# Performance work log

Measured on AMD Instinct MI355X. Metric: run time of the kernel, lower is better.

## Reference

```python
import jax, jax.numpy as jnp
import numpy as np

H_HEADS = 16
STATE_N = 64

def setup_inputs() -> dict:
    key = jax.random.key(0)
    ks = jax.random.split(key, 9)
    B, T, D = 2, 1024, 1024
    H, ch, N = H_HEADS, D // H_HEADS, STATE_N
    inp = jax.random.normal(ks[0], (B, T, D), dtype=jnp.float32)
    # lin_logA params scaled so exp(cumsum(logA)) stays bounded (decaying state)
    W_logA = jax.random.normal(ks[1], (H, 1, ch), dtype=jnp.float32) * 0.01
    b_logA = jnp.full((H, 1), -0.05, dtype=jnp.float32)
    W_XBC = jax.random.normal(ks[3], (H, ch + 2 * N, ch), dtype=jnp.float32) * (1.0 / np.sqrt(ch))
    b_XBC = jax.random.normal(ks[4], (H, ch + 2 * N), dtype=jnp.float32) * 0.02
    W_gate = jax.random.normal(ks[5], (H, ch, ch), dtype=jnp.float32) * (1.0 / np.sqrt(ch))
    b_gate = jax.random.normal(ks[6], (H, ch), dtype=jnp.float32) * 0.02
    W_out = jax.random.normal(ks[7], (D, D), dtype=jnp.float32) * (1.0 / np.sqrt(D))
    b_out = jax.random.normal(ks[8], (D,), dtype=jnp.float32) * 0.02
    return {"inp": inp, "W_logA": W_logA, "b_logA": b_logA, "W_XBC": W_XBC,
            "b_XBC": b_XBC, "W_gate": W_gate, "b_gate": b_gate,
            "W_out": W_out, "b_out": b_out}

def _mamba2_forward(inp, W_logA, b_logA, W_XBC, b_XBC, W_gate, b_gate, W_out, b_out):
    B, T, D = inp.shape
    H, N = H_HEADS, STATE_N
    ch = D // H
    x = inp.reshape(B, T, H, ch)  # B,T,H,ch
    # MultiheadLinear: matmul((H,out,in), x[...,None]) + bias
    logA = jnp.einsum('hoc,bthc->btho', W_logA, x)[..., 0] + b_logA[:, 0]  # B,T,H
    XBC = jax.nn.silu(jnp.einsum('hoc,bthc->btho', W_XBC, x) + b_XBC)     # B,T,H,ch+2N
    X = XBC[..., :ch]                 # B,T,H,ch
    Bm = XBC[..., ch:ch + N]          # B,T,H,N
    Cm = XBC[..., ch + N:]            # B,T,H,N
    # quadratic SSM: A_ss[b,h,i,j] = exp(cum[i]-cum[j]) for j<=i else 0
    cum = jnp.cumsum(jnp.swapaxes(logA, 1, 2), axis=-1)  # B,H,T
    diff = cum[..., :, None] - cum[..., None, :]          # B,H,T,T
    causal = jnp.tril(jnp.ones((T, T), dtype=bool))
    A_ss = jnp.where(causal, jnp.exp(jnp.where(causal, diff, 0.0)), 0.0)  # B,H,T,T
    G = jnp.einsum('bihn,bjhn->bhij', Cm, Bm)             # B,H,T,T (C_i . B_j)
    Y = jnp.einsum('bhij,bjhc->bihc', A_ss * G, X)        # B,T,H,ch
    gate = jnp.einsum('hoc,bthc->btho', W_gate, x) + b_gate
    Yg = (gate * Y).reshape(B, T, D)
    return Yg @ W_out.T + b_out

def reference(inp, W_logA, b_logA, W_XBC, b_XBC, W_gate, b_gate, W_out, b_out):
    return _mamba2_forward(inp, W_logA, b_logA, W_XBC, b_XBC, W_gate, b_gate, W_out, b_out)
```

## Files before the change

kernel.cpp:

```cpp
#include <hip/hip_runtime.h>

typedef unsigned int   u32;
typedef unsigned short u16;
typedef __attribute__((ext_vector_type(8))) short bf16x8;
typedef __attribute__((ext_vector_type(4))) float f32x4;

__device__ __forceinline__ float bfs(u16 u) {
  union { u32 i; float f; } v; v.i = ((u32)u) << 16; return v.f;
}
__device__ __forceinline__ u16 f2bf(float f) {
  union { float f; u32 i; } v; v.f = f;
  u32 r = v.i + 0x7fffu + ((v.i >> 16) & 1u);
  return (u16)(r >> 16);
}
__device__ __forceinline__ ushort4 f2bf4(float4 v) {
  ushort4 p; p.x = f2bf(v.x); p.y = f2bf(v.y); p.z = f2bf(v.z); p.w = f2bf(v.w);
  return p;
}

__global__ __launch_bounds__(256) void k_proj(
    const float* __restrict__ inp,
    const float* __restrict__ W_XBC,  const float* __restrict__ b_XBC,
    const float* __restrict__ W_gate, const float* __restrict__ b_gate,
    const float* __restrict__ W_logA, const float* __restrict__ b_logA,
    u16* __restrict__ XsT, u16* __restrict__ Bms, u16* __restrict__ Cms,
    u16* __restrict__ gates, float* __restrict__ logAs)
{
  int tt = blockIdx.x, h = blockIdx.y;
  int tid = threadIdx.x;
  int w = tid >> 6, l = tid & 63, q = l >> 4, lr = l & 15;
  int m0 = tt * 64;
  int b = m0 >> 10, tl0 = m0 & 1023;
  int bh = b * 16 + h;

  __shared__ u16 Xt[64][72];
  __shared__ u16 Wt[256][72];
  __shared__ float wl[64];

  if (tid < 64) wl[tid] = W_logA[h * 64 + tid];
#pragma unroll
  for (int i = 0; i < 4; ++i) {
    int f = tid + 256 * i; int r = f >> 4, cq = f & 15;
    float4 xv = *(const float4*)(inp + (size_t)(m0 + r) * 1024 + h * 64 + 4 * cq);
    *(ushort4*)&Xt[r][4 * cq] = f2bf4(xv);
  }
#pragma unroll
  for (int i = 0; i < 16; ++i) {
    int f = tid + 256 * i; int r = f >> 4, cq = f & 15;
    const float* wsrc = (r < 192) ? (W_XBC + ((size_t)h * 192 + r) * 64)
                                  : (W_gate + ((size_t)h * 64 + (r - 192)) * 64);
    *(ushort4*)&Wt[r][4 * cq] = f2bf4(*(const float4*)(wsrc + 4 * cq));
  }
  __syncthreads();

  bf16x8 af[4][2];
#pragma unroll
  for (int rt = 0; rt < 4; ++rt) {
    af[rt][0] = *(const bf16x8*)&Xt[16 * rt + lr][q * 8];
    af[rt][1] = *(const bf16x8*)&Xt[16 * rt + lr][32 + q * 8];
  }

  f32x4 acc[4][4];
#pragma unroll
  for (int rt = 0; rt < 4; ++rt)
#pragma unroll
    for (int ct = 0; ct < 4; ++ct) acc[rt][ct] = (f32x4){0.f, 0.f, 0.f, 0.f};

#pragma unroll
  for (int ct = 0; ct < 4; ++ct) {
    bf16x8 b0 = *(const bf16x8*)&Wt[64 * w + 16 * ct + lr][q * 8];
    bf16x8 b1 = *(const bf16x8*)&Wt[64 * w + 16 * ct + lr][32 + q * 8];
#pragma unroll
    for (int rt = 0; rt < 4; ++rt) {
      acc[rt][ct] = __builtin_amdgcn_mfma_f32_16x16x32_bf16(af[rt][0], b0, acc[rt][ct], 0, 0, 0);
      acc[rt][ct] = __builtin_amdgcn_mfma_f32_16x16x32_bf16(af[rt][1], b1, acc[rt][ct], 0, 0, 0);
    }
  }

  if (tid < 64) {
    float a = b_logA[h];
#pragma unroll 16
    for (int k = 0; k < 64; ++k) a += bfs(Xt[tid][k]) * wl[k];
    logAs[(size_t)bh * 1024 + tl0 + tid] = a;
  }

  if (w == 0) {
#pragma unroll
    for (int ct = 0; ct < 4; ++ct) {
      int n = 16 * ct + lr;
      float bias = b_XBC[h * 192 + n];
#pragma unroll
      for (int rt = 0; rt < 4; ++rt) {
        float4 v;
#pragma unroll
        for (int r = 0; r < 4; ++r) {
          float s = acc[rt][ct][r] + bias;
          (&v.x)[r] = s / (1.f + __expf(-s));
        }
        *(ushort4*)(XsT + ((size_t)bh * 64 + n) * 1024 + tl0 + 16 * rt + q * 4) = f2bf4(v);
      }
    }
  } else if (w < 3) {
    u16* dst = (w == 1) ? Bms : Cms;
    int nbase = h * 192 + 64 * w;
#pragma unroll
    for (int ct = 0; ct < 4; ++ct) {
      int n = 16 * ct + lr;
      float bias = b_XBC[nbase + n];
#pragma unroll
      for (int rt = 0; rt < 4; ++rt)
#pragma unroll
        for (int r = 0; r < 4; ++r) {
          int tloc = tl0 + 16 * rt + q * 4 + r;
          float s = acc[rt][ct][r] + bias;
          s = s / (1.f + __expf(-s));
          dst[((size_t)bh * 1024 + tloc) * 64 + n] = f2bf(s);
        }
    }
  } else {
#pragma unroll
    for (int ct = 0; ct < 4; ++ct) {
      int n = 16 * ct + lr;
      float bias = b_gate[h * 64 + n];
#pragma unroll
      for (int rt = 0; rt < 4; ++rt)
#pragma unroll
        for (int r = 0; r < 4; ++r) {
          int tg = m0 + 16 * rt + q * 4 + r;
          gates[((size_t)tg * 16 + h) * 64 + n] = f2bf(acc[rt][ct][r] + bias);
        }
    }
  }
}

__global__ __launch_bounds__(1024) void k_scan(
    const float* __restrict__ logAs, float* __restrict__ rowexp,
    float* __restrict__ colexp)
{
  int bh = blockIdx.x;
  int t = threadIdx.x;
  int wv = t >> 6, ln = t & 63;
  __shared__ float wsum[16];
  float v = logAs[(size_t)bh * 1024 + t];
#pragma unroll
  for (int off = 1; off < 64; off <<= 1) {
    float n = __shfl_up(v, off, 64);
    if (ln >= off) v += n;
  }
  if (ln == 63) wsum[wv] = v;
  __syncthreads();
  if (wv == 0) {
    float s = (ln < 16) ? wsum[ln] : 0.f;
#pragma unroll
    for (int off = 1; off < 16; off <<= 1) {
      float n = __shfl_up(s, off, 64);
      if (ln >= off) s += n;
    }
    if (ln < 16) wsum[ln] = s;
  }
  __syncthreads();
  if (wv > 0) v += wsum[wv - 1];
  rowexp[(size_t)bh * 1024 + t] = __expf(v);
  colexp[(size_t)bh * 1024 + t] = __expf(-v);
}

__global__ __launch_bounds__(256) void k_wconv(
    const float* __restrict__ Wout, u16* __restrict__ WoutB)
{
  int i = blockIdx.x * 256 + threadIdx.x;
  float4 v = ((const float4*)Wout)[i];
  ((ushort4*)WoutB)[i] = f2bf4(v);
}

__global__ __launch_bounds__(256) void k_ssm(
    const u16* __restrict__ XsT, const u16* __restrict__ Bms, const u16* __restrict__ Cms,
    const float* __restrict__ rowexp, const float* __restrict__ colexp,
    const u16* __restrict__ gates, u16* __restrict__ Yg)
{
  int g = blockIdx.x >> 5;
  int bh = blockIdx.x & 31;
  int it = (g & 1) ? (g >> 1) : (15 - (g >> 1));
  int b = bh >> 4, h = bh & 15;

  const u16* Xb = XsT + (size_t)bh * 64 * 1024;
  const u16* Bb = Bms + (size_t)bh * 1024 * 64;
  const u16* Cb = Cms + (size_t)bh * 1024 * 64;

  int tid = threadIdx.x;
  int w = tid >> 6, l = tid & 63, q = l >> 4, lr = l & 15;

  __shared__ u16 Cts[64][72];
  __shared__ u16 Bts[64][72];
  __shared__ u16 Xts[64][72];
  __shared__ u16 Sts[64][72];
  __shared__ float ref_[64], cef[64];

  int i0 = it * 64;
#pragma unroll
  for (int i = 0; i < 4; ++i) {
    int f = tid + 256 * i; int r = f >> 4, cq = f & 15;
    *(ushort4*)&Cts[r][4 * cq] = *(const ushort4*)(Cb + (size_t)(i0 + r) * 64 + 4 * cq);
  }
  if (tid < 64) ref_[tid] = rowexp[(size_t)bh * 1024 + i0 + tid];
  __syncthreads();

  bf16x8 ca0 = *(const bf16x8*)&Cts[16 * w + lr][q * 8];
  bf16x8 ca1 = *(const bf16x8*)&Cts[16 * w + lr][32 + q * 8];

  f32x4 acc[4];
#pragma unroll
  for (int ct = 0; ct < 4; ++ct) acc[ct] = (f32x4){0.f, 0.f, 0.f, 0.f};

  ushort4 pb[4], px[4]; float pce = 0.f;
#pragma unroll
  for (int i = 0; i < 4; ++i) {
    int f = tid + 256 * i; int r = f >> 4, cq = f & 15;
    pb[i] = *(const ushort4*)(Bb + (size_t)r * 64 + 4 * cq);
    px[i] = *(const ushort4*)(Xb + (size_t)r * 1024 + 4 * cq);
  }
  if (tid < 64) pce = colexp[(size_t)bh * 1024 + tid];

  for (int jt = 0; jt <= it; ++jt) {
    __syncthreads();
#pragma unroll
    for (int i = 0; i < 4; ++i) {
      int f = tid + 256 * i; int r = f >> 4, cq = f & 15;
      *(ushort4*)&Bts[r][4 * cq] = pb[i];
      *(ushort4*)&Xts[r][4 * cq] = px[i];
    }
    if (tid < 64) cef[tid] = pce;
    __syncthreads();

    if (jt < it) {
      int j1 = (jt + 1) * 64;
#pragma unroll
      for (int i = 0; i < 4; ++i) {
        int f = tid + 256 * i; int r = f >> 4, cq = f & 15;
        pb[i] = *(const ushort4*)(Bb + (size_t)(j1 + r) * 64 + 4 * cq);
        px[i] = *(const ushort4*)(Xb + (size_t)r * 1024 + j1 + 4 * cq);
      }
      if (tid < 64) pce = colexp[(size_t)bh * 1024 + j1 + tid];
    }

    bool diag = (jt == it);
#pragma unroll
    for (int ct = 0; ct < 4; ++ct) {
      f32x4 s = (f32x4){0.f, 0.f, 0.f, 0.f};
      bf16x8 b0 = *(const bf16x8*)&Bts[16 * ct + lr][q * 8];
      bf16x8 b1 = *(const bf16x8*)&Bts[16 * ct + lr][32 + q * 8];
      s = __builtin_amdgcn_mfma_f32_16x16x32_bf16(ca0, b0, s, 0, 0, 0);
      s = __builtin_amdgcn_mfma_f32_16x16x32_bf16(ca1, b1, s, 0, 0, 0);
      int jl = 16 * ct + lr;
      float cj = cef[jl];
#pragma unroll
      for (int r = 0; r < 4; ++r) {
        int il = 16 * w + q * 4 + r;
        float v = (diag && jl > il) ? 0.f : s[r] * ref_[il] * cj;
        Sts[il][jl] = f2bf(v);
      }
    }

    bf16x8 sa0 = *(const bf16x8*)&Sts[16 * w + lr][q * 8];
    bf16x8 sa1 = *(const bf16x8*)&Sts[16 * w + lr][32 + q * 8];
#pragma unroll
    for (int ct = 0; ct < 4; ++ct) {
      bf16x8 x0 = *(const bf16x8*)&Xts[16 * ct + lr][q * 8];
      bf16x8 x1 = *(const bf16x8*)&Xts[16 * ct + lr][32 + q * 8];
      acc[ct] = __builtin_amdgcn_mfma_f32_16x16x32_bf16(sa0, x0, acc[ct], 0, 0, 0);
      acc[ct] = __builtin_amdgcn_mfma_f32_16x16x32_bf16(sa1, x1, acc[ct], 0, 0, 0);
    }
  }

#pragma unroll
  for (int ct = 0; ct < 4; ++ct) {
    int c = 16 * ct + lr;
#pragma unroll
    for (int r = 0; r < 4; ++r) {
      int tg = i0 + 16 * w + q * 4 + r;
      size_t row = (size_t)(b * 1024 + tg);
      float gt = bfs(gates[(row * 16 + h) * 64 + c]);
      Yg[row * 1024 + h * 64 + c] = f2bf(acc[ct][r] * gt);
    }
  }
}

__global__ __launch_bounds__(512) void k_out(
    const u16* __restrict__ Yg, const u16* __restrict__ WoutB,
    const float* __restrict__ bout, float* __restrict__ out)
{
  int bm = blockIdx.x, bn = blockIdx.y;
  int tid = threadIdx.x;
  int w = tid >> 6, l = tid & 63, q = l >> 4, lr = l & 15;
  int m0 = bm * 128, d0 = bn * 64;

  __shared__ u16 Yt[128][72];
  __shared__ u16 Wt[64][72];

  f32x4 acc[4];
#pragma unroll
  for (int ct = 0; ct < 4; ++ct) acc[ct] = (f32x4){0.f, 0.f, 0.f, 0.f};

  ushort4 py[4], pw[2];
#pragma unroll
  for (int i = 0; i < 4; ++i) {
    int f = tid + 512 * i; int r = f >> 4, cq = f & 15;
    py[i] = *(const ushort4*)(Yg + (size_t)(m0 + r) * 1024 + 4 * cq);
  }
#pragma unroll
  for (int i = 0; i < 2; ++i) {
    int f = tid + 512 * i; int r = f >> 4, cq = f & 15;
    pw[i] = *(const ushort4*)(WoutB + (size_t)(d0 + r) * 1024 + 4 * cq);
  }

  for (int kt = 0; kt < 16; ++kt) {
    __syncthreads();
#pragma unroll
    for (int i = 0; i < 4; ++i) {
      int f = tid + 512 * i; int r = f >> 4, cq = f & 15;
      *(ushort4*)&Yt[r][4 * cq] = py[i];
    }
#pragma unroll
    for (int i = 0; i < 2; ++i) {
      int f = tid + 512 * i; int r = f >> 4, cq = f & 15;
      *(ushort4*)&Wt[r][4 * cq] = pw[i];
    }
    __syncthreads();

    if (kt < 15) {
      int k1 = (kt + 1) * 64;
#pragma unroll
      for (int i = 0; i < 4; ++i) {
        int f = tid + 512 * i; int r = f >> 4, cq = f & 15;
        py[i] = *(const ushort4*)(Yg + (size_t)(m0 + r) * 1024 + k1 + 4 * cq);
      }
#pragma unroll
      for (int i = 0; i < 2; ++i) {
        int f = tid + 512 * i; int r = f >> 4, cq = f & 15;
        pw[i] = *(const ushort4*)(WoutB + (size_t)(d0 + r) * 1024 + k1 + 4 * cq);
      }
    }

    bf16x8 a0 = *(const bf16x8*)&Yt[16 * w + lr][q * 8];
    bf16x8 a1 = *(const bf16x8*)&Yt[16 * w + lr][32 + q * 8];
#pragma unroll
    for (int ct = 0; ct < 4; ++ct) {
      bf16x8 b0 = *(const bf16x8*)&Wt[16 * ct + lr][q * 8];
      bf16x8 b1 = *(const bf16x8*)&Wt[16 * ct + lr][32 + q * 8];
      acc[ct] = __builtin_amdgcn_mfma_f32_16x16x32_bf16(a0, b0, acc[ct], 0, 0, 0);
      acc[ct] = __builtin_amdgcn_mfma_f32_16x16x32_bf16(a1, b1, acc[ct], 0, 0, 0);
    }
  }

#pragma unroll
  for (int ct = 0; ct < 4; ++ct) {
    int d = d0 + 16 * ct + lr;
    float bo = bout[d];
#pragma unroll
    for (int r = 0; r < 4; ++r) {
      int m = m0 + 16 * w + q * 4 + r;
      out[(size_t)m * 1024 + d] = acc[ct][r] + bo;
    }
  }
}

extern "C" void kernel_launch(void* const* d_in, const int* in_sizes, int n_in,
                              void* d_out, int out_size, void* d_ws, size_t ws_size,
                              hipStream_t stream)
{
  const float* inp   = (const float*)d_in[0];
  const float* WlogA = (const float*)d_in[1];
  const float* blogA = (const float*)d_in[2];
  const float* WXBC  = (const float*)d_in[3];
  const float* bXBC  = (const float*)d_in[4];
  const float* Wgate = (const float*)d_in[5];
  const float* bgate = (const float*)d_in[6];
  const float* Wout  = (const float*)d_in[7];
  const float* bout  = (const float*)d_in[8];
  float* out = (float*)d_out;

  const size_t SZ = (size_t)2 * 16 * 1024 * 64;
  float* logAs  = (float*)d_ws;
  float* rowexp = logAs + 32768;
  float* colexp = rowexp + 32768;
  u16* base16  = (u16*)(colexp + 32768);
  u16* XsT   = base16;
  u16* Bms   = XsT + SZ;
  u16* Cms   = Bms + SZ;
  u16* gates = Cms + SZ;
  u16* Yg    = gates + SZ;
  u16* WoutB = Yg + SZ;

  k_proj<<<dim3(32, 16), 256, 0, stream>>>(inp, WXBC, bXBC, Wgate, bgate,
                                           WlogA, blogA, XsT, Bms, Cms, gates, logAs);
  k_scan<<<32, 1024, 0, stream>>>(logAs, rowexp, colexp);
  k_wconv<<<1024, 256, 0, stream>>>(Wout, WoutB);
  k_ssm<<<dim3(512), 256, 0, stream>>>(XsT, Bms, Cms, rowexp, colexp, gates, Yg);
  k_out<<<dim3(16, 16), 512, 0, stream>>>(Yg, WoutB, bout, out);
}
```

Before: 128.9 us.

## Replace quadratic SSM with chunked state-passing scan (intra-chunk plus inter-chunk states)

Replaces the quadratic causal attention-style SSM loop over all previous chunks with a chunked formulation. Per-chunk states B^T·(colexp·X) are computed, prefix-summed across chunks, and then each chunk combines a diagonal-block term with C·H_prev scaled by rowexp. k_proj also writes a transposed copy of B, and the W_out bf16 conversion is folded into the scan kernel to save a launch. This removes the O(T^2) work and the load imbalance of the triangular loop, at the cost of two extra launches, an fp32 state buffer, a serial 16-step prefix kernel, and bf16 rounding of states that may grow from the unbounded colexp factor.

```diff
diff --git a/kernel.cpp b/kernel.cpp
--- a/kernel.cpp
+++ b/kernel.cpp
@@ -23,8 +23,8 @@
     const float* __restrict__ W_XBC,  const float* __restrict__ b_XBC,
     const float* __restrict__ W_gate, const float* __restrict__ b_gate,
     const float* __restrict__ W_logA, const float* __restrict__ b_logA,
-    u16* __restrict__ XsT, u16* __restrict__ Bms, u16* __restrict__ Cms,
-    u16* __restrict__ gates, float* __restrict__ logAs)
+    u16* __restrict__ XsT, u16* __restrict__ Bms, u16* __restrict__ BmsT,
+    u16* __restrict__ Cms, u16* __restrict__ gates, float* __restrict__ logAs)
 {
   int tt = blockIdx.x, h = blockIdx.y;
   int tid = threadIdx.x;
@@ -100,13 +100,34 @@
         *(ushort4*)(XsT + ((size_t)bh * 64 + n) * 1024 + tl0 + 16 * rt + q * 4) = f2bf4(v);
       }
     }
-  } else if (w < 3) {
-    u16* dst = (w == 1) ? Bms : Cms;
-    int nbase = h * 192 + 64 * w;
+  } else if (w == 1) {
 #pragma unroll
     for (int ct = 0; ct < 4; ++ct) {
       int n = 16 * ct + lr;
-      float bias = b_XBC[nbase + n];
+      float bias = b_XBC[h * 192 + 64 + n];
+#pragma unroll
+      for (int rt = 0; rt < 4; ++rt) {
+        float4 v;
+#pragma unroll
+        for (int r = 0; r < 4; ++r) {
+          float s = acc[rt][ct][r] + bias;
+          (&v.x)[r] = s / (1.f + __expf(-s));
+        }
+        ushort4 pv = f2bf4(v);
+        *(ushort4*)(BmsT + ((size_t)bh * 64 + n) * 1024 + tl0 + 16 * rt + q * 4) = pv;
+        u16 vs[4] = {pv.x, pv.y, pv.z, pv.w};
+#pragma unroll
+        for (int r = 0; r < 4; ++r) {
+          int tloc = tl0 + 16 * rt + q * 4 + r;
+          Bms[((size_t)bh * 1024 + tloc) * 64 + n] = vs[r];
+        }
+      }
+    }
+  } else if (w == 2) {
+#pragma unroll
+    for (int ct = 0; ct < 4; ++ct) {
+      int n = 16 * ct + lr;
+      float bias = b_XBC[h * 192 + 128 + n];
 #pragma unroll
       for (int rt = 0; rt < 4; ++rt)
 #pragma unroll
@@ -114,7 +135,7 @@
           int tloc = tl0 + 16 * rt + q * 4 + r;
           float s = acc[rt][ct][r] + bias;
           s = s / (1.f + __expf(-s));
-          dst[((size_t)bh * 1024 + tloc) * 64 + n] = f2bf(s);
+          Cms[((size_t)bh * 1024 + tloc) * 64 + n] = f2bf(s);
         }
     }
   } else {
@@ -135,7 +156,8 @@
 
 __global__ __launch_bounds__(1024) void k_scan(
     const float* __restrict__ logAs, float* __restrict__ rowexp,
-    float* __restrict__ colexp)
+    float* __restrict__ colexp,
+    const float* __restrict__ Wout, u16* __restrict__ WoutB)
 {
   int bh = blockIdx.x;
   int t = threadIdx.x;
@@ -162,113 +184,162 @@
   if (wv > 0) v += wsum[wv - 1];
   rowexp[(size_t)bh * 1024 + t] = __expf(v);
   colexp[(size_t)bh * 1024 + t] = __expf(-v);
-}
-
-__global__ __launch_bounds__(256) void k_wconv(
-    const float* __restrict__ Wout, u16* __restrict__ WoutB)
-{
-  int i = blockIdx.x * 256 + threadIdx.x;
-  float4 v = ((const float4*)Wout)[i];
-  ((ushort4*)WoutB)[i] = f2bf4(v);
-}
-
-__global__ __launch_bounds__(256) void k_ssm(
+
+  int gtid = bh * 1024 + t;
+#pragma unroll
+  for (int i = 0; i < 8; ++i) {
+    int idx = gtid + 32768 * i;
+    float4 wv4 = ((const float4*)Wout)[idx];
+    ((ushort4*)WoutB)[idx] = f2bf4(wv4);
+  }
+}
+
+__global__ __launch_bounds__(256) void k_state(
+    const u16* __restrict__ XsT, const u16* __restrict__ BmsT,
+    const float* __restrict__ colexp, float* __restrict__ G)
+{
+  int jt = blockIdx.x, bh = blockIdx.y;
+  int tid = threadIdx.x;
+  int w = tid >> 6, l = tid & 63, q = l >> 4, lr = l & 15;
+  int j0 = jt * 64;
+
+  __shared__ u16 Bt[64][72];
+  __shared__ u16 Xt[64][72];
+
+#pragma unroll
+  for (int i = 0; i < 4; ++i) {
+    int f = tid + 256 * i; int r = f >> 4, cq = f & 15;
+    *(ushort4*)&Bt[r][4 * cq] =
+        *(const ushort4*)(BmsT + ((size_t)bh * 64 + r) * 1024 + j0 + 4 * cq);
+    ushort4 xv = *(const ushort4*)(XsT + ((size_t)bh * 64 + r) * 1024 + j0 + 4 * cq);
+    float4 ce = *(const float4*)(colexp + (size_t)bh * 1024 + j0 + 4 * cq);
+    float4 sv;
+    sv.x = bfs(xv.x) * ce.x; sv.y = bfs(xv.y) * ce.y;
+    sv.z = bfs(xv.z) * ce.z; sv.w = bfs(xv.w) * ce.w;
+    *(ushort4*)&Xt[r][4 * cq] = f2bf4(sv);
+  }
+  __syncthreads();
+
+  bf16x8 a0 = *(const bf16x8*)&Bt[16 * w + lr][q * 8];
+  bf16x8 a1 = *(const bf16x8*)&Bt[16 * w + lr][32 + q * 8];
+
+  f32x4 acc[4];
+#pragma unroll
+  for (int ct = 0; ct < 4; ++ct) acc[ct] = (f32x4){0.f, 0.f, 0.f, 0.f};
+#pragma unroll
+  for (int ct = 0; ct < 4; ++ct) {
+    bf16x8 b0 = *(const bf16x8*)&Xt[16 * ct + lr][q * 8];
+    bf16x8 b1 = *(const bf16x8*)&Xt[16 * ct + lr][32 + q * 8];
+    acc[ct] = __builtin_amdgcn_mfma_f32_16x16x32_bf16(a0, b0, acc[ct], 0, 0, 0);
+    acc[ct] = __builtin_amdgcn_mfma_f32_16x16x32_bf16(a1, b1, acc[ct], 0, 0, 0);
+  }
+
+  float* Gt = G + ((size_t)bh * 16 + jt) * 4096;
+#pragma unroll
+  for (int ct = 0; ct < 4; ++ct)
+#pragma unroll
+    for (int r = 0; r < 4; ++r)
+      Gt[(16 * w + q * 4 + r) * 64 + 16 * ct + lr] = acc[ct][r];
+}
+
+__global__ __launch_bounds__(1024) void k_prefix(
+    const float* __restrict__ G, u16* __restrict__ HpreT)
+{
+  int bh = blockIdx.x;
+  int tid = threadIdx.x;
+  __shared__ float buf[64][65];
+  float h[4] = {0.f, 0.f, 0.f, 0.f};
+  for (int it = 0; it < 16; ++it) {
+    size_t base = ((size_t)bh * 16 + it) * 4096;
+#pragma unroll
+    for (int k = 0; k < 4; ++k) {
+      int e = tid + 1024 * k;
+      buf[e >> 6][e & 63] = h[k];
+    }
+    __syncthreads();
+#pragma unroll
+    for (int k = 0; k < 4; ++k) {
+      int e = tid + 1024 * k;
+      int c = e >> 6, n = e & 63;
+      HpreT[base + e] = f2bf(buf[n][c]);
+      h[k] += G[base + e];
+    }
+    __syncthreads();
+  }
+}
+
+__global__ __launch_bounds__(256) void k_ssm2(
     const u16* __restrict__ XsT, const u16* __restrict__ Bms, const u16* __restrict__ Cms,
     const float* __restrict__ rowexp, const float* __restrict__ colexp,
-    const u16* __restrict__ gates, u16* __restrict__ Yg)
-{
-  int g = blockIdx.x >> 5;
-  int bh = blockIdx.x & 31;
-  int it = (g & 1) ? (g >> 1) : (15 - (g >> 1));
+    const u16* __restrict__ HpreT, const u16* __restrict__ gates, u16* __restrict__ Yg)
+{
+  int it = blockIdx.x, bh = blockIdx.y;
   int b = bh >> 4, h = bh & 15;
-
-  const u16* Xb = XsT + (size_t)bh * 64 * 1024;
-  const u16* Bb = Bms + (size_t)bh * 1024 * 64;
-  const u16* Cb = Cms + (size_t)bh * 1024 * 64;
-
   int tid = threadIdx.x;
   int w = tid >> 6, l = tid & 63, q = l >> 4, lr = l & 15;
+  int i0 = it * 64;
 
   __shared__ u16 Cts[64][72];
   __shared__ u16 Bts[64][72];
   __shared__ u16 Xts[64][72];
   __shared__ u16 Sts[64][72];
+  __shared__ u16 HTt[64][72];
   __shared__ float ref_[64], cef[64];
 
-  int i0 = it * 64;
+  const u16* Cb = Cms + (size_t)bh * 1024 * 64;
+  const u16* Bb = Bms + (size_t)bh * 1024 * 64;
+  const u16* Xb = XsT + (size_t)bh * 64 * 1024;
+  const u16* Hb = HpreT + ((size_t)bh * 16 + it) * 4096;
+
 #pragma unroll
   for (int i = 0; i < 4; ++i) {
     int f = tid + 256 * i; int r = f >> 4, cq = f & 15;
     *(ushort4*)&Cts[r][4 * cq] = *(const ushort4*)(Cb + (size_t)(i0 + r) * 64 + 4 * cq);
-  }
-  if (tid < 64) ref_[tid] = rowexp[(size_t)bh * 1024 + i0 + tid];
+    *(ushort4*)&Bts[r][4 * cq] = *(const ushort4*)(Bb + (size_t)(i0 + r) * 64 + 4 * cq);
+    *(ushort4*)&Xts[r][4 * cq] = *(const ushort4*)(Xb + (size_t)r * 1024 + i0 + 4 * cq);
+    *(ushort4*)&HTt[r][4 * cq] = *(const ushort4*)(Hb + r * 64 + 4 * cq);
+  }
+  if (tid < 64) {
+    ref_[tid] = rowexp[(size_t)bh * 1024 + i0 + tid];
+    cef[tid]  = colexp[(size_t)bh * 1024 + i0 + tid];
+  }
   __syncthreads();
 
   bf16x8 ca0 = *(const bf16x8*)&Cts[16 * w + lr][q * 8];
   bf16x8 ca1 = *(const bf16x8*)&Cts[16 * w + lr][32 + q * 8];
 
-  f32x4 acc[4];
-#pragma unroll
-  for (int ct = 0; ct < 4; ++ct) acc[ct] = (f32x4){0.f, 0.f, 0.f, 0.f};
-
-  ushort4 pb[4], px[4]; float pce = 0.f;
-#pragma unroll
-  for (int i = 0; i < 4; ++i) {
-    int f = tid + 256 * i; int r = f >> 4, cq = f & 15;
-    pb[i] = *(const ushort4*)(Bb + (size_t)r * 64 + 4 * cq);
-    px[i] = *(const ushort4*)(Xb + (size_t)r * 1024 + 4 * cq);
-  }
-  if (tid < 64) pce = colexp[(size_t)bh * 1024 + tid];
-
-  for (int jt = 0; jt <= it; ++jt) {
-    __syncthreads();
-#pragma unroll
-    for (int i = 0; i < 4; ++i) {
-      int f = tid + 256 * i; int r = f >> 4, cq = f & 15;
-      *(ushort4*)&Bts[r][4 * cq] = pb[i];
-      *(ushort4*)&Xts[r][4 * cq] = px[i];
-    }
-    if (tid < 64) cef[tid] = pce;
-    __syncthreads();
-
-    if (jt < it) {
-      int j1 = (jt + 1) * 64;
-#pragma unroll
-      for (int i = 0; i < 4; ++i) {
-        int f = tid + 256 * i; int r = f >> 4, cq = f & 15;
-        pb[i] = *(const ushort4*)(Bb + (size_t)(j1 + r) * 64 + 4 * cq);
-        px[i] = *(const ushort4*)(Xb + (size_t)r * 1024 + j1 + 4 * cq);
-      }
-      if (tid < 64) pce = colexp[(size_t)bh * 1024 + j1 + tid];
-    }
-
-    bool diag = (jt == it);
-#pragma unroll
-    for (int ct = 0; ct < 4; ++ct) {
-      f32x4 s = (f32x4){0.f, 0.f, 0.f, 0.f};
-      bf16x8 b0 = *(const bf16x8*)&Bts[16 * ct + lr][q * 8];
-      bf16x8 b1 = *(const bf16x8*)&Bts[16 * ct + lr][32 + q * 8];
-      s = __builtin_amdgcn_mfma_f32_16x16x32_bf16(ca0, b0, s, 0, 0, 0);
-      s = __builtin_amdgcn_mfma_f32_16x16x32_bf16(ca1, b1, s, 0, 0, 0);
-      int jl = 16 * ct + lr;
-      float cj = cef[jl];
-#pragma unroll
-      for (int r = 0; r < 4; ++r) {
-        int il = 16 * w + q * 4 + r;
-        float v = (diag && jl > il) ? 0.f : s[r] * ref_[il] * cj;
-        Sts[il][jl] = f2bf(v);
-      }
-    }
-
-    bf16x8 sa0 = *(const bf16x8*)&Sts[16 * w + lr][q * 8];
-    bf16x8 sa1 = *(const bf16x8*)&Sts[16 * w + lr][32 + q * 8];
-#pragma unroll
-    for (int ct = 0; ct < 4; ++ct) {
-      bf16x8 x0 = *(const bf16x8*)&Xts[16 * ct + lr][q * 8];
-      bf16x8 x1 = *(const bf16x8*)&Xts[16 * ct + lr][32 + q * 8];
-      acc[ct] = __builtin_amdgcn_mfma_f32_16x16x32_bf16(sa0, x0, acc[ct], 0, 0, 0);
-      acc[ct] = __builtin_amdgcn_mfma_f32_16x16x32_bf16(sa1, x1, acc[ct], 0, 0, 0);
-    }
+#pragma unroll
+  for (int ct = 0; ct < 4; ++ct) {
+    f32x4 s = (f32x4){0.f, 0.f, 0.f, 0.f};
+    bf16x8 b0 = *(const bf16x8*)&Bts[16 * ct + lr][q * 8];
+    bf16x8 b1 = *(const bf16x8*)&Bts[16 * ct + lr][32 + q * 8];
+    s = __builtin_amdgcn_mfma_f32_16x16x32_bf16(ca0, b0, s, 0, 0, 0);
+    s = __builtin_amdgcn_mfma_f32_16x16x32_bf16(ca1, b1, s, 0, 0, 0);
+    int jl = 16 * ct + lr;
+    float cj = cef[jl];
+#pragma unroll
+    for (int r = 0; r < 4; ++r) {
+      int il = 16 * w + q * 4 + r;
+      float v = (jl > il) ? 0.f : s[r] * ref_[il] * cj;
+      Sts[il][jl] = f2bf(v);
+    }
+  }
+
+  bf16x8 sa0 = *(const bf16x8*)&Sts[16 * w + lr][q * 8];
+  bf16x8 sa1 = *(const bf16x8*)&Sts[16 * w + lr][32 + q * 8];
+  f32x4 accd[4], acco[4];
+#pragma unroll
+  for (int ct = 0; ct < 4; ++ct) {
+    accd[ct] = (f32x4){0.f, 0.f, 0.f, 0.f};
+    acco[ct] = (f32x4){0.f, 0.f, 0.f, 0.f};
+    bf16x8 x0 = *(const bf16x8*)&Xts[16 * ct + lr][q * 8];
+    bf16x8 x1 = *(const bf16x8*)&Xts[16 * ct + lr][32 + q * 8];
+    accd[ct] = __builtin_amdgcn_mfma_f32_16x16x32_bf16(sa0, x0, accd[ct], 0, 0, 0);
+    accd[ct] = __builtin_amdgcn_mfma_f32_16x16x32_bf16(sa1, x1, accd[ct], 0, 0, 0);
+    bf16x8 h0 = *(const bf16x8*)&HTt[16 * ct + lr][q * 8];
+    bf16x8 h1 = *(const bf16x8*)&HTt[16 * ct + lr][32 + q * 8];
+    acco[ct] = __builtin_amdgcn_mfma_f32_16x16x32_bf16(ca0, h0, acco[ct], 0, 0, 0);
+    acco[ct] = __builtin_amdgcn_mfma_f32_16x16x32_bf16(ca1, h1, acco[ct], 0, 0, 0);
   }
 
 #pragma unroll
@@ -276,10 +347,12 @@
     int c = 16 * ct + lr;
 #pragma unroll
     for (int r = 0; r < 4; ++r) {
-      int tg = i0 + 16 * w + q * 4 + r;
+      int il = 16 * w + q * 4 + r;
+      int tg = i0 + il;
       size_t row = (size_t)(b * 1024 + tg);
+      float y = accd[ct][r] + ref_[il] * acco[ct][r];
       float gt = bfs(gates[(row * 16 + h) * 64 + c]);
-      Yg[row * 1024 + h * 64 + c] = f2bf(acc[ct][r] * gt);
+      Yg[row * 1024 + h * 64 + c] = f2bf(y * gt);
     }
   }
 }
@@ -382,18 +455,24 @@
   float* logAs  = (float*)d_ws;
   float* rowexp = logAs + 32768;
   float* colexp = rowexp + 32768;
-  u16* base16  = (u16*)(colexp + 32768);
+  float* G      = colexp + 32768;
+  u16* base16  = (u16*)(G + (size_t)32 * 16 * 4096);
   u16* XsT   = base16;
   u16* Bms   = XsT + SZ;
-  u16* Cms   = Bms + SZ;
+  u16* BmsT  = Bms + SZ;
+  u16* Cms   = BmsT + SZ;
   u16* gates = Cms + SZ;
   u16* Yg    = gates + SZ;
   u16* WoutB = Yg + SZ;
+  u16* HpreT = WoutB + 1024 * 1024;
 
   k_proj<<<dim3(32, 16), 256, 0, stream>>>(inp, WXBC, bXBC, Wgate, bgate,
-                                           WlogA, blogA, XsT, Bms, Cms, gates, logAs);
-  k_scan<<<32, 1024, 0, stream>>>(logAs, rowexp, colexp);
-  k_wconv<<<1024, 256, 0, stream>>>(Wout, WoutB);
-  k_ssm<<<dim3(512), 256, 0, stream>>>(XsT, Bms, Cms, rowexp, colexp, gates, Yg);
+                                           WlogA, blogA, XsT, Bms, BmsT, Cms,
+                                           gates, logAs);
+  k_scan<<<32, 1024, 0, stream>>>(logAs, rowexp, colexp, Wout, WoutB);
+  k_state<<<dim3(16, 32), 256, 0, stream>>>(XsT, BmsT, colexp, G);
+  k_prefix<<<32, 1024, 0, stream>>>(G, HpreT);
+  k_ssm2<<<dim3(16, 32), 256, 0, stream>>>(XsT, Bms, Cms, rowexp, colexp,
+                                           HpreT, gates, Yg);
   k_out<<<dim3(16, 16), 512, 0, stream>>>(Yg, WoutB, bout, out);
 }
```

New measurement: 128.4 us. About the same (-0.4%).

## Replace quadratic SSM with chunked state-passing scan and fuse projection prologue

Applied to the files above, without the earlier changes.

The full causal quadratic SSM loop over all earlier chunks is replaced by a chunked formulation. The projection kernel now computes chunk-local cumulative decays. It also computes per-chunk state contributions (X·diag(decay)·Bᵀ) with MFMA. A small kernel then recurrently propagates inter-chunk states, and the SSM kernel only does the diagonal block plus a C·H correction. The separate scan and Wout-conversion kernels are folded into the projection kernel, and B/C/gates are written in transposed layouts through shared memory for coalesced stores. This cuts the SSM work from quadratic to linear in sequence length, in exchange for an extra state buffer, a bf16-quantized state, and more work in the projection kernel.

```diff
diff --git a/kernel.cpp b/kernel.cpp
--- a/kernel.cpp
+++ b/kernel.cpp
@@ -23,8 +23,10 @@
     const float* __restrict__ W_XBC,  const float* __restrict__ b_XBC,
     const float* __restrict__ W_gate, const float* __restrict__ b_gate,
     const float* __restrict__ W_logA, const float* __restrict__ b_logA,
-    u16* __restrict__ XsT, u16* __restrict__ Bms, u16* __restrict__ Cms,
-    u16* __restrict__ gates, float* __restrict__ logAs)
+    const float* __restrict__ Wout, u16* __restrict__ WoutB,
+    u16* __restrict__ XsT, u16* __restrict__ BmsT, u16* __restrict__ CmsT,
+    u16* __restrict__ gatesP, float* __restrict__ lexp, float* __restrict__ linv,
+    float* __restrict__ decArr, float* __restrict__ G)
 {
   int tt = blockIdx.x, h = blockIdx.y;
   int tid = threadIdx.x;
@@ -32,10 +34,19 @@
   int m0 = tt * 64;
   int b = m0 >> 10, tl0 = m0 & 1023;
   int bh = b * 16 + h;
+  int jt = tt & 15;
 
   __shared__ u16 Xt[64][72];
   __shared__ u16 Wt[256][72];
   __shared__ float wl[64];
+  __shared__ float sg[64];
+
+  {
+    int fid = h * 32 + tt;
+    const float4* src = (const float4*)Wout + (size_t)fid * 512;
+    ushort4* dst = (ushort4*)WoutB + (size_t)fid * 512;
+    for (int i = tid; i < 512; i += 256) dst[i] = f2bf4(src[i]);
+  }
 
   if (tid < 64) wl[tid] = W_logA[h * 64 + tid];
 #pragma unroll
@@ -47,9 +58,9 @@
 #pragma unroll
   for (int i = 0; i < 16; ++i) {
     int f = tid + 256 * i; int r = f >> 4, cq = f & 15;
-    const float* wsrc = (r < 192) ? (W_XBC + ((size_t)h * 192 + r) * 64)
-                                  : (W_gate + ((size_t)h * 64 + (r - 192)) * 64);
-    *(ushort4*)&Wt[r][4 * cq] = f2bf4(*(const float4*)(wsrc + 4 * cq));
+    const float* ws = (r < 192) ? (W_XBC + ((size_t)h * 192 + r) * 64)
+                                : (W_gate + ((size_t)h * 64 + (r - 192)) * 64);
+    *(ushort4*)&Wt[r][4 * cq] = f2bf4(*(const float4*)(ws + 4 * cq));
   }
   __syncthreads();
 
@@ -81,194 +92,206 @@
     float a = b_logA[h];
 #pragma unroll 16
     for (int k = 0; k < 64; ++k) a += bfs(Xt[tid][k]) * wl[k];
-    logAs[(size_t)bh * 1024 + tl0 + tid] = a;
-  }
-
-  if (w == 0) {
+    float lv = a;
+#pragma unroll
+    for (int off = 1; off < 64; off <<= 1) {
+      float n = __shfl_up(lv, off, 64);
+      if (tid >= off) lv += n;
+    }
+    float L = __shfl(lv, 63, 64);
+    sg[tid] = __expf(L - lv);
+    lexp[(size_t)bh * 1024 + tl0 + tid] = __expf(lv);
+    linv[(size_t)bh * 1024 + tl0 + tid] = __expf(-lv);
+    if (tid == 63) decArr[bh * 16 + jt] = __expf(L);
+  }
+
+  if (w < 3) {
 #pragma unroll
     for (int ct = 0; ct < 4; ++ct) {
-      int n = 16 * ct + lr;
-      float bias = b_XBC[h * 192 + n];
-#pragma unroll
-      for (int rt = 0; rt < 4; ++rt) {
-        float4 v;
+      float bias = b_XBC[h * 192 + 64 * w + 16 * ct + lr];
+#pragma unroll
+      for (int rt = 0; rt < 4; ++rt)
 #pragma unroll
         for (int r = 0; r < 4; ++r) {
           float s = acc[rt][ct][r] + bias;
-          (&v.x)[r] = s / (1.f + __expf(-s));
+          acc[rt][ct][r] = s / (1.f + __expf(-s));
         }
-        *(ushort4*)(XsT + ((size_t)bh * 64 + n) * 1024 + tl0 + 16 * rt + q * 4) = f2bf4(v);
-      }
-    }
-  } else if (w < 3) {
-    u16* dst = (w == 1) ? Bms : Cms;
-    int nbase = h * 192 + 64 * w;
+    }
+  } else {
 #pragma unroll
     for (int ct = 0; ct < 4; ++ct) {
-      int n = 16 * ct + lr;
-      float bias = b_XBC[nbase + n];
+      float bias = b_gate[h * 64 + 16 * ct + lr];
 #pragma unroll
       for (int rt = 0; rt < 4; ++rt)
 #pragma unroll
+        for (int r = 0; r < 4; ++r) acc[rt][ct][r] += bias;
+    }
+  }
+  __syncthreads();
+
+  {
+    u16* T = &Wt[64 * w][0];
+#pragma unroll
+    for (int ct = 0; ct < 4; ++ct)
+#pragma unroll
+      for (int rt = 0; rt < 4; ++rt)
+#pragma unroll
         for (int r = 0; r < 4; ++r) {
-          int tloc = tl0 + 16 * rt + q * 4 + r;
-          float s = acc[rt][ct][r] + bias;
-          s = s / (1.f + __expf(-s));
-          dst[((size_t)bh * 1024 + tloc) * 64 + n] = f2bf(s);
+          int t = 16 * rt + 4 * q + r, n = 16 * ct + lr;
+          u16 v = f2bf(acc[rt][ct][r]);
+          if (w < 3) T[n * 72 + t] = v;
+          else       T[t * 72 + n] = v;
         }
-    }
-  } else {
-#pragma unroll
-    for (int ct = 0; ct < 4; ++ct) {
-      int n = 16 * ct + lr;
-      float bias = b_gate[h * 64 + n];
-#pragma unroll
-      for (int rt = 0; rt < 4; ++rt)
-#pragma unroll
-        for (int r = 0; r < 4; ++r) {
-          int tg = m0 + 16 * rt + q * 4 + r;
-          gates[((size_t)tg * 16 + h) * 64 + n] = f2bf(acc[rt][ct][r] + bias);
-        }
-    }
-  }
-}
-
-__global__ __launch_bounds__(1024) void k_scan(
-    const float* __restrict__ logAs, float* __restrict__ rowexp,
-    float* __restrict__ colexp)
+  }
+  __syncthreads();
+
+  {
+#pragma unroll
+    for (int i = 0; i < 16; ++i) {
+      int s = l + 64 * i; int row = s >> 4, cq = s & 15;
+      ushort4 v = *(ushort4*)&Wt[64 * w + row][4 * cq];
+      if (w == 0)
+        *(ushort4*)(XsT + ((size_t)bh * 64 + row) * 1024 + tl0 + 4 * cq) = v;
+      else if (w == 1)
+        *(ushort4*)(BmsT + ((size_t)bh * 64 + row) * 1024 + tl0 + 4 * cq) = v;
+      else if (w == 2)
+        *(ushort4*)(CmsT + ((size_t)bh * 64 + row) * 1024 + tl0 + 4 * cq) = v;
+      else
+        *(ushort4*)(gatesP + ((size_t)bh * 1024 + tl0 + row) * 64 + 4 * cq) = v;
+    }
+  }
+
+  {
+    bf16x8 a0r = *(const bf16x8*)&Wt[16 * w + lr][q * 8];
+    bf16x8 a1r = *(const bf16x8*)&Wt[16 * w + lr][32 + q * 8];
+    bf16x8 a0, a1;
+#pragma unroll
+    for (int jj = 0; jj < 8; ++jj) {
+      a0[jj] = (short)f2bf(bfs((u16)a0r[jj]) * sg[q * 8 + jj]);
+      a1[jj] = (short)f2bf(bfs((u16)a1r[jj]) * sg[32 + q * 8 + jj]);
+    }
+    f32x4 gacc[4];
+#pragma unroll
+    for (int nt = 0; nt < 4; ++nt) {
+      gacc[nt] = (f32x4){0.f, 0.f, 0.f, 0.f};
+      bf16x8 bb0 = *(const bf16x8*)&Wt[64 + 16 * nt + lr][q * 8];
+      bf16x8 bb1 = *(const bf16x8*)&Wt[64 + 16 * nt + lr][32 + q * 8];
+      gacc[nt] = __builtin_amdgcn_mfma_f32_16x16x32_bf16(a0, bb0, gacc[nt], 0, 0, 0);
+      gacc[nt] = __builtin_amdgcn_mfma_f32_16x16x32_bf16(a1, bb1, gacc[nt], 0, 0, 0);
+    }
+    float* Gt = G + ((size_t)bh * 16 + jt) * 4096;
+#pragma unroll
+    for (int nt = 0; nt < 4; ++nt)
+#pragma unroll
+      for (int r = 0; r < 4; ++r)
+        Gt[(16 * w + 4 * q + r) * 64 + 16 * nt + lr] = gacc[nt][r];
+  }
+}
+
+__global__ __launch_bounds__(1024) void k_mid(
+    const float* __restrict__ G, const float* __restrict__ decArr,
+    u16* __restrict__ HpreT)
 {
-  int bh = blockIdx.x;
-  int t = threadIdx.x;
-  int wv = t >> 6, ln = t & 63;
-  __shared__ float wsum[16];
-  float v = logAs[(size_t)bh * 1024 + t];
-#pragma unroll
-  for (int off = 1; off < 64; off <<= 1) {
-    float n = __shfl_up(v, off, 64);
-    if (ln >= off) v += n;
-  }
-  if (ln == 63) wsum[wv] = v;
+  int cc = blockIdx.x, bh = blockIdx.y;
+  int tid = threadIdx.x;
+  int e = cc * 1024 + tid;
+  __shared__ float dsm[16];
+  if (tid < 16) dsm[tid] = decArr[bh * 16 + tid];
   __syncthreads();
-  if (wv == 0) {
-    float s = (ln < 16) ? wsum[ln] : 0.f;
-#pragma unroll
-    for (int off = 1; off < 16; off <<= 1) {
-      float n = __shfl_up(s, off, 64);
-      if (ln >= off) s += n;
-    }
-    if (ln < 16) wsum[ln] = s;
-  }
-  __syncthreads();
-  if (wv > 0) v += wsum[wv - 1];
-  rowexp[(size_t)bh * 1024 + t] = __expf(v);
-  colexp[(size_t)bh * 1024 + t] = __expf(-v);
-}
-
-__global__ __launch_bounds__(256) void k_wconv(
-    const float* __restrict__ Wout, u16* __restrict__ WoutB)
+  const float* Gb = G + (size_t)bh * 16 * 4096 + e;
+  float g[16];
+#pragma unroll
+  for (int jtl = 0; jtl < 16; ++jtl) g[jtl] = Gb[(size_t)jtl * 4096];
+  u16* Hb = HpreT + (size_t)bh * 16 * 4096 + e;
+  float hst = 0.f;
+#pragma unroll
+  for (int jtl = 0; jtl < 16; ++jtl) {
+    Hb[(size_t)jtl * 4096] = f2bf(hst);
+    hst = dsm[jtl] * hst + g[jtl];
+  }
+}
+
+__global__ __launch_bounds__(256) void k_ssm2(
+    const u16* __restrict__ XsT, const u16* __restrict__ BmsT,
+    const u16* __restrict__ CmsT,
+    const float* __restrict__ lexp, const float* __restrict__ linv,
+    const u16* __restrict__ HpreT, const u16* __restrict__ gatesP,
+    u16* __restrict__ Yg)
 {
-  int i = blockIdx.x * 256 + threadIdx.x;
-  float4 v = ((const float4*)Wout)[i];
-  ((ushort4*)WoutB)[i] = f2bf4(v);
-}
-
-__global__ __launch_bounds__(256) void k_ssm(
-    const u16* __restrict__ XsT, const u16* __restrict__ Bms, const u16* __restrict__ Cms,
-    const float* __restrict__ rowexp, const float* __restrict__ colexp,
-    const u16* __restrict__ gates, u16* __restrict__ Yg)
-{
-  int g = blockIdx.x >> 5;
-  int bh = blockIdx.x & 31;
-  int it = (g & 1) ? (g >> 1) : (15 - (g >> 1));
+  int it = blockIdx.x, bh = blockIdx.y;
   int b = bh >> 4, h = bh & 15;
-
-  const u16* Xb = XsT + (size_t)bh * 64 * 1024;
-  const u16* Bb = Bms + (size_t)bh * 1024 * 64;
-  const u16* Cb = Cms + (size_t)bh * 1024 * 64;
-
   int tid = threadIdx.x;
   int w = tid >> 6, l = tid & 63, q = l >> 4, lr = l & 15;
+  int i0 = it * 64;
 
   __shared__ u16 Cts[64][72];
   __shared__ u16 Bts[64][72];
   __shared__ u16 Xts[64][72];
+  __shared__ u16 HTt[64][72];
+  __shared__ u16 Gts[64][72];
   __shared__ u16 Sts[64][72];
   __shared__ float ref_[64], cef[64];
 
-  int i0 = it * 64;
+  const u16* Xb  = XsT  + (size_t)bh * 64 * 1024;
+  const u16* BbT = BmsT + (size_t)bh * 64 * 1024;
+  const u16* CbT = CmsT + (size_t)bh * 64 * 1024;
+  const u16* Hb  = HpreT + ((size_t)bh * 16 + it) * 4096;
+  const u16* Gb  = gatesP + ((size_t)bh * 1024 + i0) * 64;
+
 #pragma unroll
   for (int i = 0; i < 4; ++i) {
     int f = tid + 256 * i; int r = f >> 4, cq = f & 15;
-    *(ushort4*)&Cts[r][4 * cq] = *(const ushort4*)(Cb + (size_t)(i0 + r) * 64 + 4 * cq);
-  }
-  if (tid < 64) ref_[tid] = rowexp[(size_t)bh * 1024 + i0 + tid];
+    *(ushort4*)&Xts[r][4 * cq] = *(const ushort4*)(Xb + (size_t)r * 1024 + i0 + 4 * cq);
+    *(ushort4*)&HTt[r][4 * cq] = *(const ushort4*)(Hb + r * 64 + 4 * cq);
+    *(ushort4*)&Gts[r][4 * cq] = *(const ushort4*)(Gb + r * 64 + 4 * cq);
+    ushort4 bv = *(const ushort4*)(BbT + (size_t)r * 1024 + i0 + 4 * cq);
+    Bts[4 * cq + 0][r] = bv.x; Bts[4 * cq + 1][r] = bv.y;
+    Bts[4 * cq + 2][r] = bv.z; Bts[4 * cq + 3][r] = bv.w;
+    ushort4 cv = *(const ushort4*)(CbT + (size_t)r * 1024 + i0 + 4 * cq);
+    Cts[4 * cq + 0][r] = cv.x; Cts[4 * cq + 1][r] = cv.y;
+    Cts[4 * cq + 2][r] = cv.z; Cts[4 * cq + 3][r] = cv.w;
+  }
+  if (tid < 64) {
+    ref_[tid] = lexp[(size_t)bh * 1024 + i0 + tid];
+    cef[tid]  = linv[(size_t)bh * 1024 + i0 + tid];
+  }
   __syncthreads();
 
   bf16x8 ca0 = *(const bf16x8*)&Cts[16 * w + lr][q * 8];
   bf16x8 ca1 = *(const bf16x8*)&Cts[16 * w + lr][32 + q * 8];
 
-  f32x4 acc[4];
-#pragma unroll
-  for (int ct = 0; ct < 4; ++ct) acc[ct] = (f32x4){0.f, 0.f, 0.f, 0.f};
-
-  ushort4 pb[4], px[4]; float pce = 0.f;
-#pragma unroll
-  for (int i = 0; i < 4; ++i) {
-    int f = tid + 256 * i; int r = f >> 4, cq = f & 15;
-    pb[i] = *(const ushort4*)(Bb + (size_t)r * 64 + 4 * cq);
-    px[i] = *(const ushort4*)(Xb + (size_t)r * 1024 + 4 * cq);
-  }
-  if (tid < 64) pce = colexp[(size_t)bh * 1024 + tid];
-
-  for (int jt = 0; jt <= it; ++jt) {
-    __syncthreads();
-#pragma unroll
-    for (int i = 0; i < 4; ++i) {
-      int f = tid + 256 * i; int r = f >> 4, cq = f & 15;
-      *(ushort4*)&Bts[r][4 * cq] = pb[i];
-      *(ushort4*)&Xts[r][4 * cq] = px[i];
-    }
-    if (tid < 64) cef[tid] = pce;
-    __syncthreads();
-
-    if (jt < it) {
-      int j1 = (jt + 1) * 64;
-#pragma unroll
-      for (int i = 0; i < 4; ++i) {
-        int f = tid + 256 * i; int r = f >> 4, cq = f & 15;
-        pb[i] = *(const ushort4*)(Bb + (size_t)(j1 + r) * 64 + 4 * cq);
-        px[i] = *(const ushort4*)(Xb + (size_t)r * 1024 + j1 + 4 * cq);
-      }
-      if (tid < 64) pce = colexp[(size_t)bh * 1024 + j1 + tid];
-    }
-
-    bool diag = (jt == it);
-#pragma unroll
-    for (int ct = 0; ct < 4; ++ct) {
-      f32x4 s = (f32x4){0.f, 0.f, 0.f, 0.f};
-      bf16x8 b0 = *(const bf16x8*)&Bts[16 * ct + lr][q * 8];
-      bf16x8 b1 = *(const bf16x8*)&Bts[16 * ct + lr][32 + q * 8];
-      s = __builtin_amdgcn_mfma_f32_16x16x32_bf16(ca0, b0, s, 0, 0, 0);
-      s = __builtin_amdgcn_mfma_f32_16x16x32_bf16(ca1, b1, s, 0, 0, 0);
-      int jl = 16 * ct + lr;
-      float cj = cef[jl];
-#pragma unroll
-      for (int r = 0; r < 4; ++r) {
-        int il = 16 * w + q * 4 + r;
-        float v = (diag && jl > il) ? 0.f : s[r] * ref_[il] * cj;
-        Sts[il][jl] = f2bf(v);
-      }
-    }
-
-    bf16x8 sa0 = *(const bf16x8*)&Sts[16 * w + lr][q * 8];
-    bf16x8 sa1 = *(const bf16x8*)&Sts[16 * w + lr][32 + q * 8];
-#pragma unroll
-    for (int ct = 0; ct < 4; ++ct) {
-      bf16x8 x0 = *(const bf16x8*)&Xts[16 * ct + lr][q * 8];
-      bf16x8 x1 = *(const bf16x8*)&Xts[16 * ct + lr][32 + q * 8];
-      acc[ct] = __builtin_amdgcn_mfma_f32_16x16x32_bf16(sa0, x0, acc[ct], 0, 0, 0);
-      acc[ct] = __builtin_amdgcn_mfma_f32_16x16x32_bf16(sa1, x1, acc[ct], 0, 0, 0);
-    }
+#pragma unroll
+  for (int ct = 0; ct < 4; ++ct) {
+    f32x4 s = (f32x4){0.f, 0.f, 0.f, 0.f};
+    bf16x8 b0 = *(const bf16x8*)&Bts[16 * ct + lr][q * 8];
+    bf16x8 b1 = *(const bf16x8*)&Bts[16 * ct + lr][32 + q * 8];
+    s = __builtin_amdgcn_mfma_f32_16x16x32_bf16(ca0, b0, s, 0, 0, 0);
+    s = __builtin_amdgcn_mfma_f32_16x16x32_bf16(ca1, b1, s, 0, 0, 0);
+    int jl = 16 * ct + lr;
+    float cj = cef[jl];
+#pragma unroll
+    for (int r = 0; r < 4; ++r) {
+      int il = 16 * w + q * 4 + r;
+      float v = (jl > il) ? 0.f : s[r] * ref_[il] * cj;
+      Sts[il][jl] = f2bf(v);
+    }
+  }
+
+  bf16x8 sa0 = *(const bf16x8*)&Sts[16 * w + lr][q * 8];
+  bf16x8 sa1 = *(const bf16x8*)&Sts[16 * w + lr][32 + q * 8];
+  f32x4 accd[4], acco[4];
+#pragma unroll
+  for (int ct = 0; ct < 4; ++ct) {
+    accd[ct] = (f32x4){0.f, 0.f, 0.f, 0.f};
+    acco[ct] = (f32x4){0.f, 0.f, 0.f, 0.f};
+    bf16x8 x0 = *(const bf16x8*)&Xts[16 * ct + lr][q * 8];
+    bf16x8 x1 = *(const bf16x8*)&Xts[16 * ct + lr][32 + q * 8];
+    accd[ct] = __builtin_amdgcn_mfma_f32_16x16x32_bf16(sa0, x0, accd[ct], 0, 0, 0);
+    accd[ct] = __builtin_amdgcn_mfma_f32_16x16x32_bf16(sa1, x1, accd[ct], 0, 0, 0);
+    bf16x8 h0 = *(const bf16x8*)&HTt[16 * ct + lr][q * 8];
+    bf16x8 h1 = *(const bf16x8*)&HTt[16 * ct + lr][32 + q * 8];
+    acco[ct] = __builtin_amdgcn_mfma_f32_16x16x32_bf16(ca0, h0, acco[ct], 0, 0, 0);
+    acco[ct] = __builtin_amdgcn_mfma_f32_16x16x32_bf16(ca1, h1, acco[ct], 0, 0, 0);
   }
 
 #pragma unroll
@@ -276,10 +299,12 @@
     int c = 16 * ct + lr;
 #pragma unroll
     for (int r = 0; r < 4; ++r) {
-      int tg = i0 + 16 * w + q * 4 + r;
+      int il = 16 * w + q * 4 + r;
+      int tg = i0 + il;
       size_t row = (size_t)(b * 1024 + tg);
-      float gt = bfs(gates[(row * 16 + h) * 64 + c]);
-      Yg[row * 1024 + h * 64 + c] = f2bf(acc[ct][r] * gt);
+      float y = accd[ct][r] + ref_[il] * acco[ct][r];
+      float gt = bfs(Gts[il][c]);
+      Yg[row * 1024 + h * 64 + c] = f2bf(y * gt);
     }
   }
 }
@@ -379,21 +404,25 @@
   float* out = (float*)d_out;
 
   const size_t SZ = (size_t)2 * 16 * 1024 * 64;
-  float* logAs  = (float*)d_ws;
-  float* rowexp = logAs + 32768;
-  float* colexp = rowexp + 32768;
-  u16* base16  = (u16*)(colexp + 32768);
-  u16* XsT   = base16;
-  u16* Bms   = XsT + SZ;
-  u16* Cms   = Bms + SZ;
-  u16* gates = Cms + SZ;
-  u16* Yg    = gates + SZ;
-  u16* WoutB = Yg + SZ;
+  float* lexp   = (float*)d_ws;
+  float* linv   = lexp + 32768;
+  float* decA   = linv + 32768;
+  float* G      = decA + 512;
+  u16* base16 = (u16*)(G + (size_t)32 * 16 * 4096);
+  u16* XsT    = base16;
+  u16* BmsT   = XsT + SZ;
+  u16* CmsT   = BmsT + SZ;
+  u16* gatesP = CmsT + SZ;
+  u16* Yg     = gatesP + SZ;
+  u16* WoutB  = Yg + SZ;
+  u16* HpreT  = WoutB + 1024 * 1024;
 
   k_proj<<<dim3(32, 16), 256, 0, stream>>>(inp, WXBC, bXBC, Wgate, bgate,
-                                           WlogA, blogA, XsT, Bms, Cms, gates, logAs);
-  k_scan<<<32, 1024, 0, stream>>>(logAs, rowexp, colexp);
-  k_wconv<<<1024, 256, 0, stream>>>(Wout, WoutB);
-  k_ssm<<<dim3(512), 256, 0, stream>>>(XsT, Bms, Cms, rowexp, colexp, gates, Yg);
+                                           WlogA, blogA, Wout, WoutB,
+                                           XsT, BmsT, CmsT, gatesP,
+                                           lexp, linv, decA, G);
+  k_mid<<<dim3(4, 32), 1024, 0, stream>>>(G, decA, HpreT);
+  k_ssm2<<<dim3(16, 32), 256, 0, stream>>>(XsT, BmsT, CmsT, lexp, linv,
+                                           HpreT, gatesP, Yg);
   k_out<<<dim3(16, 16), 512, 0, stream>>>(Yg, WoutB, bout, out);
 }
```

Result: faster. 118.4 us (-8.1%).
